# Performance work log

Hardware: AMD Instinct MI355X
Metric: run time of the kernel (lower is better)

Reference implementation:

```python
import jax, jax.numpy as jnp
import numpy as np

B, T, D, H = 2, 2048, 1024, 16

def setup_inputs() -> dict:
    key = jax.random.key(0)
    k0, k1, k2, k3 = jax.random.split(key, 4)
    s = 0.02
    return {
        "x": jax.random.normal(k0, (B, T, D), dtype=jnp.float32),
        "Wqkv": jax.random.normal(k1, (3 * D, D), dtype=jnp.float32) * s,
        "Wout": jax.random.normal(k2, (D, D), dtype=jnp.float32) * s,
        "bout": jax.random.normal(k3, (D,), dtype=jnp.float32) * s,
    }

def reference(x, Wqkv, Wout, bout):
    b, t, d = x.shape
    h = H
    dh = d // h
    qkv = x @ Wqkv.T  # [b,t,3d]
    q, k, v = jnp.split(qkv, 3, axis=-1)
    def merge_heads(z):
        return z.reshape(b, t, h, dh).transpose(0, 2, 1, 3)  # [b,h,t,dh]
    q, k, v = map(merge_heads, (q, k, v))
    scale = dh ** -0.5
    dots = jnp.einsum('bhid,bhjd->bhij', q, k) * scale  # [b,h,t,t]
    causal_mask = jnp.triu(jnp.ones((t, t), dtype=bool), 1)
    dots = jnp.where(causal_mask, -jnp.inf, dots)
    attn = jax.nn.softmax(dots, axis=-1)
    out = jnp.einsum('bhij,bhjd->bhid', attn, v)  # [b,h,t,dh]
    out = out.transpose(0, 2, 1, 3).reshape(b, t, d)
    return out @ Wout.T + bout
```

## Files before the change

### kernel.cpp

```cpp
#include <hip/hip_runtime.h>
#include <hip/hip_bf16.h>
#include <math.h>

typedef __bf16 bf16x8 __attribute__((ext_vector_type(8)));
typedef float f32x4 __attribute__((ext_vector_type(4)));
typedef unsigned short u16;
typedef unsigned int u32;
typedef u32 u32x2 __attribute__((ext_vector_type(2)));

#define EXP2F(x) __builtin_amdgcn_exp2f(x)

constexpr int Bz = 2, T = 2048, D = 1024, H = 16;
constexpr int M = Bz * T;
constexpr int NQKV = 3 * D;
constexpr float SCALE2 = 0.125f * 1.44269504089f;

#define GLD_LDS16(g, l) __builtin_amdgcn_global_load_lds( \
    (__attribute__((address_space(1))) void*)(g),          \
    (__attribute__((address_space(3))) void*)(l), 16, 0, 0)

__global__ void cvt_all_kernel(const float* __restrict__ x,
                               const float* __restrict__ wq,
                               const float* __restrict__ wo,
                               u16* __restrict__ xb, u16* __restrict__ wqb,
                               u16* __restrict__ wob) {
  constexpr int NX = M * D / 4;
  constexpr int NQ = NQKV * D / 4;
  constexpr int NW = D * D / 4;
  constexpr int TOT = NX + NQ + NW;
  int i = blockIdx.x * blockDim.x + threadIdx.x;
  int stride = gridDim.x * blockDim.x;
  for (; i < TOT; i += stride) {
    const float4* src;
    u16* dst;
    int j;
    if (i < NX) { src = (const float4*)x; dst = xb; j = i; }
    else if (i < NX + NQ) { src = (const float4*)wq; dst = wqb; j = i - NX; }
    else { src = (const float4*)wo; dst = wob; j = i - NX - NQ; }
    float4 f = src[j];
    ushort4 u;
    u.x = __builtin_bit_cast(u16, (__bf16)f.x);
    u.y = __builtin_bit_cast(u16, (__bf16)f.y);
    u.z = __builtin_bit_cast(u16, (__bf16)f.z);
    u.w = __builtin_bit_cast(u16, (__bf16)f.w);
    ((ushort4*)dst)[j] = u;
  }
}

template <bool FP32OUT, bool QSCALE>
__global__ __launch_bounds__(256, 2)
void gemm_bt(const u16* __restrict__ A, const u16* __restrict__ Bm,
             u16* __restrict__ outb, float* __restrict__ outf,
             const float* __restrict__ bias, int K, int ldc) {
  __shared__ __align__(16) u16 sA[128 * 64];
  __shared__ __align__(16) u16 sB[128 * 64];
  const int tid = threadIdx.x;
  const int lane = tid & 63;
  const int wid = tid >> 6;
  const int wr = wid >> 1, wc = wid & 1;

  const int nwg = gridDim.x * gridDim.y;
  const int flat = blockIdx.y * gridDim.x + blockIdx.x;
  const int cpx = nwg >> 3;
  const int swz = (flat & 7) * cpx + (flat >> 3);
  const int bx = swz % gridDim.x;
  const int by = swz / gridDim.x;

  const int row0 = by * 128;
  const int col0 = bx * 128;

  f32x4 acc[4][4];
#pragma unroll
  for (int m = 0; m < 4; ++m)
#pragma unroll
    for (int n = 0; n < 4; ++n) acc[m][n] = (f32x4){0.f, 0.f, 0.f, 0.f};

  const int nk = K >> 6;
  for (int kt = 0; kt < nk; ++kt) {
    const int k0 = kt << 6;
#pragma unroll
    for (int i = 0; i < 4; ++i) {
      int off = i * 4096 + tid * 16;
      int r = off >> 7;
      int cs = (off >> 4) & 7;
      int c = cs ^ (r & 7);
      const u16* ga = A + (size_t)(row0 + r) * K + k0 + c * 8;
      const u16* gb = Bm + (size_t)(col0 + r) * K + k0 + c * 8;
      u16* la = sA + (i * 4096 + (tid & ~63) * 16) / 2;
      u16* lb = sB + (i * 4096 + (tid & ~63) * 16) / 2;
      GLD_LDS16(ga, la);
      GLD_LDS16(gb, lb);
    }
    __syncthreads();
#pragma unroll
    for (int kk = 0; kk < 2; ++kk) {
      bf16x8 af[4], bfv[4];
#pragma unroll
      for (int m = 0; m < 4; ++m) {
        int r = wr * 64 + m * 16 + (lane & 15);
        int cs = (kk * 4 + (lane >> 4)) ^ (r & 7);
        af[m] = *(const bf16x8*)(sA + r * 64 + cs * 8);
      }
#pragma unroll
      for (int n = 0; n < 4; ++n) {
        int r = wc * 64 + n * 16 + (lane & 15);
        int cs = (kk * 4 + (lane >> 4)) ^ (r & 7);
        bfv[n] = *(const bf16x8*)(sB + r * 64 + cs * 8);
      }
#pragma unroll
      for (int m = 0; m < 4; ++m)
#pragma unroll
        for (int n = 0; n < 4; ++n)
          acc[m][n] = __builtin_amdgcn_mfma_f32_16x16x32_bf16(
              af[m], bfv[n], acc[m][n], 0, 0, 0);
    }
    __syncthreads();
  }

  const int orow0 = row0 + wr * 64;
  const int ocol0 = col0 + wc * 64;
#pragma unroll
  for (int m = 0; m < 4; ++m)
#pragma unroll
    for (int n = 0; n < 4; ++n)
#pragma unroll
      for (int j = 0; j < 4; ++j) {
        int rr = orow0 + m * 16 + (lane >> 4) * 4 + j;
        int cc = ocol0 + n * 16 + (lane & 15);
        if (FP32OUT) {
          outf[(size_t)rr * ldc + cc] = acc[m][n][j] + bias[cc];
        } else {
          float v = acc[m][n][j];
          if (QSCALE && cc < D) v *= SCALE2;
          outb[(size_t)rr * ldc + cc] = __builtin_bit_cast(u16, (__bf16)v);
        }
      }
}

__global__ __launch_bounds__(256, 4)
void flash_kernel(const u16* __restrict__ qkv, u16* __restrict__ attn_out) {
  __shared__ __align__(16) u16 sK[2][64 * 64];
  __shared__ __align__(16) u16 sVt[64 * 72];
  __shared__ __align__(16) u16 sP[4][16][72];

  const int tid = threadIdx.x;
  const int lane = tid & 63;
  const int l15 = lane & 15;
  const int hi = lane >> 4;
  const int w = tid >> 6;
  const int bh = blockIdx.x;
  const int b = bh >> 4, h = bh & 15;
  const int qt = (gridDim.y - 1) - blockIdx.y;
  const int q0 = qt * 64;
  const int nv = qt + 1;

  const size_t base = (size_t)b * T * 3072;
  const u16* qp = qkv + base + 0 * 1024 + h * 64;
  const u16* kp = qkv + base + 1 * 1024 + h * 64;
  const u16* vp = qkv + base + 2 * 1024 + h * 64;

  ushort4 vr[2][2];
  auto stageK = [&](u16* dst, int kt) {
#pragma unroll
    for (int i = 0; i < 2; ++i) {
      int off = i * 4096 + tid * 16;
      int r = off >> 7;
      int cs = (off >> 4) & 7;
      int c = cs ^ (r & 7);
      GLD_LDS16(kp + (size_t)(kt * 64 + r) * 3072 + c * 8,
                dst + (i * 4096 + (tid & ~63) * 16) / 2);
    }
  };
  auto loadV = [&](int kt) {
#pragma unroll
    for (int i = 0; i < 2; ++i) {
      const u16* gsrc = vp + (size_t)(kt * 64 + lane) * 3072 + (i * 4 + w) * 8;
      vr[i][0] = ((const ushort4*)gsrc)[0];
      vr[i][1] = ((const ushort4*)gsrc)[1];
    }
  };
  auto writeV = [&]() {
#pragma unroll
    for (int i = 0; i < 2; ++i) {
      int c = i * 4 + w;
      sVt[(c * 8 + 0) * 72 + lane] = vr[i][0].x;
      sVt[(c * 8 + 1) * 72 + lane] = vr[i][0].y;
      sVt[(c * 8 + 2) * 72 + lane] = vr[i][0].z;
      sVt[(c * 8 + 3) * 72 + lane] = vr[i][0].w;
      sVt[(c * 8 + 4) * 72 + lane] = vr[i][1].x;
      sVt[(c * 8 + 5) * 72 + lane] = vr[i][1].y;
      sVt[(c * 8 + 6) * 72 + lane] = vr[i][1].z;
      sVt[(c * 8 + 7) * 72 + lane] = vr[i][1].w;
    }
  };

  bf16x8 qf[2];
#pragma unroll
  for (int kk = 0; kk < 2; ++kk)
    qf[kk] = *(const bf16x8*)(qp + (size_t)(q0 + w * 16 + l15) * 3072 +
                              kk * 32 + hi * 8);

  f32x4 o_acc[4];
#pragma unroll
  for (int n = 0; n < 4; ++n) o_acc[n] = (f32x4){0.f, 0.f, 0.f, 0.f};
  float l_run = 0.f;

  stageK(sK[0], 0);
  loadV(0);
  writeV();
  __syncthreads();

  for (int v = 0; v < nv; ++v) {
    const int cur = v & 1;
    const int k0 = v * 64;
    if (v + 1 < nv) {
      stageK(sK[cur ^ 1], v + 1);
      loadV(v + 1);
    }

    bf16x8 kf[2][4];
#pragma unroll
    for (int kk = 0; kk < 2; ++kk)
#pragma unroll
      for (int n = 0; n < 4; ++n) {
        int rk = n * 16 + l15;
        int cs = (kk * 4 + hi) ^ (rk & 7);
        kf[kk][n] = *(const bf16x8*)(&sK[cur][rk * 64 + cs * 8]);
      }
    bf16x8 vf[2][4];
#pragma unroll
    for (int ks = 0; ks < 2; ++ks)
#pragma unroll
      for (int n = 0; n < 4; ++n)
        vf[ks][n] = *(const bf16x8*)(
            &sVt[(n * 16 + l15) * 72 + ks * 32 + hi * 8]);

    f32x4 sc[4];
#pragma unroll
    for (int n = 0; n < 4; ++n) sc[n] = (f32x4){0.f, 0.f, 0.f, 0.f};
    __builtin_amdgcn_s_setprio(1);
#pragma unroll
    for (int kk = 0; kk < 2; ++kk)
#pragma unroll
      for (int n = 0; n < 4; ++n)
        sc[n] = __builtin_amdgcn_mfma_f32_16x16x32_bf16(kf[kk][n], qf[kk],
                                                        sc[n], 0, 0, 0);
    __builtin_amdgcn_s_setprio(0);

    const bool diag = (v == nv - 1);
    const int qrow = q0 + w * 16 + l15;
    if (diag) {
#pragma unroll
      for (int n = 0; n < 4; ++n)
#pragma unroll
        for (int r = 0; r < 4; ++r) {
          int kpos = k0 + n * 16 + hi * 4 + r;
          if (kpos > qrow) sc[n][r] = -INFINITY;
        }
    }

    float psum = 0.f;
    bf16x8 pf0, pf1;
#pragma unroll
    for (int n = 0; n < 2; ++n) {
      float p0 = EXP2F(sc[n][0]);
      float p1 = EXP2F(sc[n][1]);
      float p2 = EXP2F(sc[n][2]);
      float p3 = EXP2F(sc[n][3]);
      psum += (p0 + p1) + (p2 + p3);
      u32x2 pw;
      pw.x = ((u32)__builtin_bit_cast(u16, (__bf16)p1) << 16) |
             __builtin_bit_cast(u16, (__bf16)p0);
      pw.y = ((u32)__builtin_bit_cast(u16, (__bf16)p3) << 16) |
             __builtin_bit_cast(u16, (__bf16)p2);
      *(u32x2*)(&sP[w][l15][n * 16 + hi * 4]) = pw;
    }
    pf0 = *(const bf16x8*)(&sP[w][l15][hi * 8]);
#pragma unroll
    for (int n = 2; n < 4; ++n) {
      float p0 = EXP2F(sc[n][0]);
      float p1 = EXP2F(sc[n][1]);
      float p2 = EXP2F(sc[n][2]);
      float p3 = EXP2F(sc[n][3]);
      psum += (p0 + p1) + (p2 + p3);
      u32x2 pw;
      pw.x = ((u32)__builtin_bit_cast(u16, (__bf16)p1) << 16) |
             __builtin_bit_cast(u16, (__bf16)p0);
      pw.y = ((u32)__builtin_bit_cast(u16, (__bf16)p3) << 16) |
             __builtin_bit_cast(u16, (__bf16)p2);
      *(u32x2*)(&sP[w][l15][n * 16 + hi * 4]) = pw;
    }
    l_run += psum;

    __builtin_amdgcn_s_setprio(1);
#pragma unroll
    for (int n = 0; n < 4; ++n)
      o_acc[n] = __builtin_amdgcn_mfma_f32_16x16x32_bf16(pf0, vf[0][n],
                                                         o_acc[n], 0, 0, 0);
    pf1 = *(const bf16x8*)(&sP[w][l15][32 + hi * 8]);
#pragma unroll
    for (int n = 0; n < 4; ++n)
      o_acc[n] = __builtin_amdgcn_mfma_f32_16x16x32_bf16(pf1, vf[1][n],
                                                         o_acc[n], 0, 0, 0);
    __builtin_amdgcn_s_setprio(0);

    if (v + 1 < nv) {
      __syncthreads();
      writeV();
      __syncthreads();
    }
  }

  l_run += __shfl_xor(l_run, 16, 64);
  l_run += __shfl_xor(l_run, 32, 64);

#pragma unroll
  for (int j = 0; j < 4; ++j) {
    float lj = __shfl(l_run, hi * 4 + j, 64);
    float inv = 1.f / lj;
    int row = q0 + w * 16 + hi * 4 + j;
#pragma unroll
    for (int n = 0; n < 4; ++n) {
      int cc = h * 64 + n * 16 + l15;
      attn_out[((size_t)b * T + row) * 1024 + cc] =
          __builtin_bit_cast(u16, (__bf16)(o_acc[n][j] * inv));
    }
  }
}

extern "C" void kernel_launch(void* const* d_in, const int* in_sizes, int n_in,
                              void* d_out, int out_size, void* d_ws,
                              size_t ws_size, hipStream_t stream) {
  (void)in_sizes; (void)n_in; (void)out_size; (void)ws_size;
  const float* x = (const float*)d_in[0];
  const float* Wqkv = (const float*)d_in[1];
  const float* Wout = (const float*)d_in[2];
  const float* bout = (const float*)d_in[3];
  float* out = (float*)d_out;

  char* ws = (char*)d_ws;
  u16* x_bf = (u16*)(ws + 0);
  u16* wqkv_bf = (u16*)(ws + 8388608);
  u16* wout_bf = (u16*)(ws + 14680064);
  u16* qkvb = (u16*)(ws + 16777216);
  u16* aout = (u16*)(ws + 41943040);

  cvt_all_kernel<<<2048, 256, 0, stream>>>(x, Wqkv, Wout, x_bf, wqkv_bf,
                                           wout_bf);

  gemm_bt<false, true><<<dim3(NQKV / 128, M / 128), 256, 0, stream>>>(
      x_bf, wqkv_bf, qkvb, nullptr, nullptr, D, NQKV);

  flash_kernel<<<dim3(Bz * H, T / 64), 256, 0, stream>>>(qkvb, aout);

  gemm_bt<true, false><<<dim3(D / 128, M / 128), 256, 0, stream>>>(
      aout, wout_bf, nullptr, out, bout, D, D);
}
```

Baseline: 102.6 us.

## Replace QKV GEMM with 256x256-tile 8-phase pipelined kernel

Adds a dedicated QKV projection GEMM that uses 256x256 tiles, 512 threads and double-buffered LDS. Global-to-LDS loads are staged in halves and interleaved with MFMA quarters across eight barrier-separated phases, with raised scheduling priority during MFMA. The aim is higher operand reuse and overlap of memory traffic with compute. The trade-off is that only 192 workgroups are launched, fewer than the CU count, and each uses large LDS and register footprints.

```diff
diff --git a/kernel.cpp b/kernel.cpp
--- a/kernel.cpp
+++ b/kernel.cpp
@@ -18,6 +18,9 @@
 #define GLD_LDS16(g, l) __builtin_amdgcn_global_load_lds( \
     (__attribute__((address_space(1))) void*)(g),          \
     (__attribute__((address_space(3))) void*)(l), 16, 0, 0)
+
+#define BARRIER() do { __builtin_amdgcn_s_barrier(); \
+                       __builtin_amdgcn_sched_barrier(0); } while (0)
 
 __global__ void cvt_all_kernel(const float* __restrict__ x,
                                const float* __restrict__ wq,
@@ -47,6 +50,160 @@
   }
 }
 
+__global__ __launch_bounds__(512, 2)
+void gemm1_8ph(const u16* __restrict__ A, const u16* __restrict__ Bm,
+               u16* __restrict__ outb) {
+  constexpr int K = 1024;
+  constexpr int LDC = NQKV;
+  __shared__ __align__(16) u16 sA[2][256 * 64];
+  __shared__ __align__(16) u16 sB[2][256 * 64];
+  const int tid = threadIdx.x;
+  const int lane = tid & 63;
+  const int l15 = lane & 15;
+  const int hi = lane >> 4;
+  const int wid = tid >> 6;
+  const int wm = wid >> 2;
+  const int wn = wid & 3;
+
+  const int nwg = gridDim.x * gridDim.y;
+  const int flat = blockIdx.y * gridDim.x + blockIdx.x;
+  const int cpx = nwg >> 3;
+  const int swz = (flat & 7) * cpx + (flat >> 3);
+  const int bx = swz % gridDim.x;
+  const int by = swz / gridDim.x;
+  const int row0 = by * 256;
+  const int col0 = bx * 256;
+
+  f32x4 acc[8][4];
+#pragma unroll
+  for (int m = 0; m < 8; ++m)
+#pragma unroll
+    for (int n = 0; n < 4; ++n) acc[m][n] = (f32x4){0.f, 0.f, 0.f, 0.f};
+
+  auto stageHalf = [&](u16* dstbuf, const u16* src, int srow0, int half,
+                       int k0) {
+#pragma unroll
+    for (int i = 0; i < 2; ++i) {
+      int off = i * 8192 + tid * 16;
+      int rl = off >> 7;
+      int r = half * 128 + rl;
+      int cs = (off >> 4) & 7;
+      int c = cs ^ (r & 7);
+      GLD_LDS16(src + (size_t)(srow0 + r) * K + k0 + c * 8,
+                dstbuf + (half * 16384 + i * 8192 + (tid & ~63) * 16) / 2);
+    }
+  };
+
+  bf16x8 af[2][4], bfr[2][4];
+  auto ldAf = [&](const u16* buf, int mh) {
+#pragma unroll
+    for (int kk = 0; kk < 2; ++kk)
+#pragma unroll
+      for (int m = 0; m < 4; ++m) {
+        int r = wm * 128 + mh * 64 + m * 16 + l15;
+        int cs = (kk * 4 + hi) ^ (r & 7);
+        af[kk][m] = *(const bf16x8*)(buf + r * 64 + cs * 8);
+      }
+  };
+  auto ldBf = [&](const u16* buf, int nh) {
+#pragma unroll
+    for (int kk = 0; kk < 2; ++kk)
+#pragma unroll
+      for (int n = 0; n < 2; ++n) {
+        int r = wn * 64 + (nh * 2 + n) * 16 + l15;
+        int cs = (kk * 4 + hi) ^ (r & 7);
+        bfr[kk][nh * 2 + n] = *(const bf16x8*)(buf + r * 64 + cs * 8);
+      }
+  };
+  auto mmaQ = [&](int mh, int nh) {
+    __builtin_amdgcn_s_setprio(1);
+#pragma unroll
+    for (int kk = 0; kk < 2; ++kk)
+#pragma unroll
+      for (int m = 0; m < 4; ++m)
+#pragma unroll
+        for (int n = 0; n < 2; ++n)
+          acc[mh * 4 + m][nh * 2 + n] = __builtin_amdgcn_mfma_f32_16x16x32_bf16(
+              af[kk][m], bfr[kk][nh * 2 + n], acc[mh * 4 + m][nh * 2 + n],
+              0, 0, 0);
+    __builtin_amdgcn_s_setprio(0);
+  };
+
+  stageHalf(sA[0], A, row0, 0, 0);
+  stageHalf(sA[0], A, row0, 1, 0);
+  stageHalf(sB[0], Bm, col0, 0, 0);
+  stageHalf(sB[0], Bm, col0, 1, 0);
+  stageHalf(sB[1], Bm, col0, 0, 64);
+  stageHalf(sB[1], Bm, col0, 1, 64);
+  asm volatile("s_waitcnt vmcnt(4)" ::: "memory");
+  BARRIER();
+
+  constexpr int ITERS = 8;
+  for (int it = 0; it < ITERS; ++it) {
+    const int t1 = 2 * it + 1;
+    const bool more = (it + 1 < ITERS);
+    const int kA = (2 * it + 2) * 64;
+    const int kB = (2 * it + 3) * 64;
+
+    ldAf(sA[0], 0);
+    ldBf(sB[0], 0);
+    stageHalf(sA[1], A, row0, 0, t1 * 64);
+    BARRIER();
+    mmaQ(0, 0);
+    BARRIER();
+    ldBf(sB[0], 1);
+    stageHalf(sA[1], A, row0, 1, t1 * 64);
+    BARRIER();
+    mmaQ(0, 1);
+    BARRIER();
+    ldAf(sA[0], 1);
+    if (more) stageHalf(sB[0], Bm, col0, 0, kA);
+    BARRIER();
+    mmaQ(1, 0);
+    BARRIER();
+    if (more) stageHalf(sB[0], Bm, col0, 1, kA);
+    BARRIER();
+    mmaQ(1, 1);
+    if (more) asm volatile("s_waitcnt vmcnt(4)" ::: "memory");
+    else      asm volatile("s_waitcnt vmcnt(0)" ::: "memory");
+    BARRIER();
+    ldAf(sA[1], 0);
+    ldBf(sB[1], 0);
+    if (more) stageHalf(sA[0], A, row0, 0, kA);
+    BARRIER();
+    mmaQ(0, 0);
+    BARRIER();
+    ldBf(sB[1], 1);
+    if (more) stageHalf(sA[0], A, row0, 1, kA);
+    BARRIER();
+    mmaQ(0, 1);
+    BARRIER();
+    ldAf(sA[1], 1);
+    if (more) stageHalf(sB[1], Bm, col0, 0, kB);
+    BARRIER();
+    mmaQ(1, 0);
+    BARRIER();
+    if (more) stageHalf(sB[1], Bm, col0, 1, kB);
+    BARRIER();
+    mmaQ(1, 1);
+    if (more) asm volatile("s_waitcnt vmcnt(4)" ::: "memory");
+    BARRIER();
+  }
+
+#pragma unroll
+  for (int mf = 0; mf < 8; ++mf)
+#pragma unroll
+    for (int nf = 0; nf < 4; ++nf)
+#pragma unroll
+      for (int j = 0; j < 4; ++j) {
+        int rr = row0 + wm * 128 + mf * 16 + hi * 4 + j;
+        int cc = col0 + wn * 64 + nf * 16 + l15;
+        float v = acc[mf][nf][j];
+        if (cc < D) v *= SCALE2;
+        outb[(size_t)rr * LDC + cc] = __builtin_bit_cast(u16, (__bf16)v);
+      }
+}
+
 template <bool FP32OUT, bool QSCALE>
 __global__ __launch_bounds__(256, 2)
 void gemm_bt(const u16* __restrict__ A, const u16* __restrict__ Bm,
@@ -348,8 +505,8 @@
   cvt_all_kernel<<<2048, 256, 0, stream>>>(x, Wqkv, Wout, x_bf, wqkv_bf,
                                            wout_bf);
 
-  gemm_bt<false, true><<<dim3(NQKV / 128, M / 128), 256, 0, stream>>>(
-      x_bf, wqkv_bf, qkvb, nullptr, nullptr, D, NQKV);
+  gemm1_8ph<<<dim3(NQKV / 256, M / 256), 512, 0, stream>>>(x_bf, wqkv_bf,
+                                                           qkvb);
 
   flash_kernel<<<dim3(Bz * H, T / 64), 256, 0, stream>>>(qkvb, aout);
 
```

Result: slower. 104.6 us (+2.0%).
